# Kernel optimization log

Hardware: AMD Instinct MI355X
Metric: run time of the kernel (lower is better)

## Reference

```python
import jax, jax.numpy as jnp
import numpy as np
import math

NUM_HEADS = 12


def setup_inputs() -> dict:
    key = jax.random.key(0)
    ks = jax.random.split(key, 9)
    R, L, B, E = 128, 512, 1, 768
    s = 1.0 / math.sqrt(E)
    return {
        "x": jax.random.normal(ks[0], (R, L, B, E), dtype=jnp.float32),
        "wq": jax.random.normal(ks[1], (E, E), dtype=jnp.float32) * s,
        "bq": jax.random.normal(ks[2], (E,), dtype=jnp.float32) * 0.02,
        "wk": jax.random.normal(ks[3], (E, E), dtype=jnp.float32) * s,
        "bk": jax.random.normal(ks[4], (E,), dtype=jnp.float32) * 0.02,
        "wv": jax.random.normal(ks[5], (E, E), dtype=jnp.float32) * s,
        "bv": jax.random.normal(ks[6], (E,), dtype=jnp.float32) * 0.02,
        "wo": jax.random.normal(ks[7], (E, E), dtype=jnp.float32) * s,
        "bo": jax.random.normal(ks[8], (E,), dtype=jnp.float32) * 0.02,
    }


def reference(x, wq, bq, wk, bk, wv, bv, wo, bo):
    # x: [num_rows, num_cols, batch, embed_dim]
    R, L, B, E = x.shape
    H = NUM_HEADS
    D = E // H
    # scaling = head_dim**-0.5 / sqrt(num_rows)  (align_scaling)
    scaling = (D ** -0.5) / math.sqrt(R)

    q = (x @ wq.T + bq).reshape(R, L, B, H, D) * scaling
    k = (x @ wk.T + bk).reshape(R, L, B, H, D)
    v = (x @ wv.T + bv).reshape(R, L, B, H, D)

    # row attention: contract over rows r and head_dim d -> logits [h, n, i, j]
    attn_weights = jnp.einsum("rinhd,rjnhd->hnij", q, k)
    attn_probs = jax.nn.softmax(attn_weights, axis=-1)

    context = jnp.einsum("hnij,rjnhd->rinhd", attn_probs, v)
    context = context.reshape(R, L, B, E)
    output = context @ wo.T + bo
    return (output, attn_probs)
```

## Files before the change

kernel.cpp:

```cpp
#include <hip/hip_runtime.h>
#include <hip/hip_bf16.h>

typedef unsigned short u16;
typedef u16   u16x4 __attribute__((ext_vector_type(4)));
typedef u16   u16x8 __attribute__((ext_vector_type(8)));
typedef short bf16x8 __attribute__((ext_vector_type(8)));
typedef float f32x4 __attribute__((ext_vector_type(4)));

#define R_    128
#define L_    512
#define E_    768
#define H_    12
#define RD_   8192
#define M_    65536
#define OUT0_N 50331648
#define PART_ 3145728

__device__ __forceinline__ u16 rne_bf16(float f) {
  unsigned u = __builtin_bit_cast(unsigned, f);
  u += 0x7FFFu + ((u >> 16) & 1u);
  return (u16)(u >> 16);
}

__device__ __forceinline__ void gload_lds16(const u16* g, u16* l) {
  __builtin_amdgcn_global_load_lds(
      (const __attribute__((address_space(1))) void*)g,
      (__attribute__((address_space(3))) void*)l, 16, 0, 0);
}

__device__ __forceinline__ int xcd_remap(int d, int nwg) {
  return (d & 7) * (nwg >> 3) + (d >> 3);
}

__device__ __forceinline__ void gemm_core(
    const u16* __restrict__ Ab, const u16* __restrict__ Bb,
    const int lda, const int ldb, const int K,
    u16* sm, f32x4 acc[4][4])
{
  const int t    = threadIdx.x;
  const int lane = t & 63;
  const int w    = t >> 6;
  const int wm   = (w >> 1) << 6;
  const int wn   = (w & 1) << 6;
  const int frow = lane & 15;

  const int srow = (w << 3) + (lane >> 3);
  const int scol = ((lane & 7) ^ (lane >> 3)) << 3;
  const u16* gA = Ab + (size_t)srow * lda + scol;
  const u16* gB = Bb + (size_t)srow * ldb + scol;
  const int stg_l = (w << 9) + (lane << 3);

#pragma unroll
  for (int j = 0; j < 4; ++j) {
    gload_lds16(gA + (size_t)(j << 5) * lda, sm + (j << 11) + stg_l);
    gload_lds16(gB + (size_t)(j << 5) * ldb, sm + 8192 + (j << 11) + stg_l);
  }

  const int nt = K >> 6;
  for (int tt = 0; tt < nt; ++tt) {
    const int cur = tt & 1;
    u16* bufc = sm + (cur << 14);
    u16* bufn = sm + ((cur ^ 1) << 14);
    __builtin_amdgcn_s_barrier();
    if (tt + 1 < nt) {
      const u16* gA1 = gA + ((size_t)(tt + 1) << 6);
      const u16* gB1 = gB + ((size_t)(tt + 1) << 6);
#pragma unroll
      for (int j = 0; j < 4; ++j) {
        gload_lds16(gA1 + (size_t)(j << 5) * lda, bufn + (j << 11) + stg_l);
        gload_lds16(gB1 + (size_t)(j << 5) * ldb, bufn + 8192 + (j << 11) + stg_l);
      }
      asm volatile("s_waitcnt vmcnt(8)" ::: "memory");
    } else {
      asm volatile("s_waitcnt vmcnt(0)" ::: "memory");
    }
    __builtin_amdgcn_s_barrier();
    const u16* sA = bufc;
    const u16* sB = bufc + 8192;
#pragma unroll
    for (int kk = 0; kk < 2; ++kk) {
      const int rdcol = (((kk << 2) + (lane >> 4)) ^ (lane & 7)) << 3;
      bf16x8 af[4], bff[4];
#pragma unroll
      for (int a = 0; a < 4; ++a)
        af[a] = *(const bf16x8*)(sA + ((wm + a * 16 + frow) << 6) + rdcol);
#pragma unroll
      for (int b = 0; b < 4; ++b)
        bff[b] = *(const bf16x8*)(sB + ((wn + b * 16 + frow) << 6) + rdcol);
#pragma unroll
      for (int a = 0; a < 4; ++a)
#pragma unroll
        for (int b = 0; b < 4; ++b)
          acc[a][b] = __builtin_amdgcn_mfma_f32_16x16x32_bf16(af[a], bff[b], acc[a][b], 0, 0, 0);
    }
  }
}

#define EPILOGUE_IDX                              \
  const int lane = threadIdx.x & 63;              \
  const int w    = threadIdx.x >> 6;              \
  const int wm   = (w >> 1) << 6;                 \
  const int wn   = (w & 1) << 6;                  \
  const int row4 = (lane >> 4) << 2;              \
  const int coll = lane & 15;

#define ACC_INIT                                  \
  f32x4 acc[4][4];                                \
  {                                               \
    f32x4 zz = {0.0f, 0.0f, 0.0f, 0.0f};          \
    _Pragma("unroll")                             \
    for (int a = 0; a < 4; ++a)                   \
      _Pragma("unroll")                           \
      for (int b = 0; b < 4; ++b) acc[a][b] = zz; \
  }

__global__ __launch_bounds__(256) void k_gemm_qkv(
    const u16* __restrict__ xbf, const u16* __restrict__ wqkv,
    const float* __restrict__ bq, const float* __restrict__ bk,
    const float* __restrict__ bv,
    u16* __restrict__ qt, u16* __restrict__ kt, u16* __restrict__ vt2,
    const float scaling)
{
  __shared__ __align__(16) u16 smem[32768];
  const int d0 = blockIdx.x + 18 * blockIdx.y;
  const int l  = xcd_remap(d0, 18 * 512);
  const int bn = l % 18;
  const int bm = l / 18;
  ACC_INIT;
  gemm_core(xbf + (size_t)bm * 128 * E_, wqkv + (size_t)bn * 128 * E_,
            E_, E_, E_, smem, acc);
  EPILOGUE_IDX;
  const int n0 = bn * 128;
  const int which = n0 / E_;
  const int c0 = n0 - which * E_;
  const float* bias = (which == 0) ? bq : (which == 1) ? bk : bv;

  if (which < 2) {
    u16* dst = (which == 0) ? qt : kt;
    const float mult = (which == 0) ? scaling : 1.0f;
#pragma unroll
    for (int a = 0; a < 4; ++a) {
#pragma unroll
      for (int b = 0; b < 4; ++b) {
        const int nl = wn + b * 16 + coll;
        const int c = c0 + nl;
        const int h = c >> 6, d = c & 63;
        const float bias_v = bias[c];
#pragma unroll
        for (int r = 0; r < 4; ++r) {
          const int m = bm * 128 + wm + a * 16 + row4 + r;
          const int rr = m >> 9, i = m & 511;
          const float v = (acc[a][b][r] + bias_v) * mult;
          dst[((size_t)(h * 512 + i) << 13) + (rr << 6) + d] = rne_bf16(v);
        }
      }
    }
  } else {
    __syncthreads();
    u16* Tr = smem;
#pragma unroll
    for (int a = 0; a < 4; ++a) {
      const int mlb = wm + a * 16 + row4;
#pragma unroll
      for (int b = 0; b < 4; ++b) {
        const int nl = wn + b * 16 + coll;
        const float bias_v = bias[c0 + nl];
        u16x4 pk;
#pragma unroll
        for (int r = 0; r < 4; ++r) pk[r] = rne_bf16(acc[a][b][r] + bias_v);
        *(u16x4*)(Tr + nl * 136 + mlb) = pk;
      }
    }
    __syncthreads();
    const int rr = (bm * 128) >> 9;
    const int j0 = (bm * 128) & 511;
    for (int idx = threadIdx.x; idx < 128 * 16; idx += 256) {
      const int nl = idx >> 4, seg = idx & 15;
      const int c = c0 + nl;
      const int h = c >> 6, d = c & 63;
      u16x8 vdat = *(const u16x8*)(Tr + nl * 136 + (seg << 3));
      *(u16x8*)(vt2 + ((size_t)((h << 13) + (rr << 6) + d) << 9) + j0 + (seg << 3)) = vdat;
    }
  }
}

__global__ __launch_bounds__(256) void k_gemm_logits(
    const u16* __restrict__ qt, const u16* __restrict__ kt,
    float* __restrict__ lgp)
{
  __shared__ __align__(16) u16 smem[32768];
  const int d0 = blockIdx.x + 4 * blockIdx.y + 16 * blockIdx.z;
  const int l  = xcd_remap(d0, 768);
  const int bm = l & 3, bn = (l >> 2) & 3;
  const int hk = l >> 4;
  const int h  = hk >> 2, ks = hk & 3;
  ACC_INIT;
  const u16* A = qt + ((size_t)h << 22) + ((size_t)bm << 20) + (ks << 11);
  const u16* B = kt + ((size_t)h << 22) + ((size_t)bn << 20) + (ks << 11);
  gemm_core(A, B, RD_, RD_, 2048, smem, acc);
  EPILOGUE_IDX;
  float* dst = lgp + ((size_t)(ks * 12 + h) << 18);
#pragma unroll
  for (int a = 0; a < 4; ++a)
#pragma unroll
    for (int b = 0; b < 4; ++b) {
      const int j = bn * 128 + wn + b * 16 + coll;
#pragma unroll
      for (int r = 0; r < 4; ++r) {
        const int i = bm * 128 + wm + a * 16 + row4 + r;
        dst[((size_t)i << 9) + j] = acc[a][b][r];
      }
    }
}

__global__ __launch_bounds__(256) void k_softmax(
    const float* __restrict__ lgp, float* __restrict__ probs,
    u16* __restrict__ pbf)
{
  const int row = blockIdx.x;
  const size_t base = (size_t)row << 9;
  const int t = threadIdx.x;
  const int lane = t & 63, w = t >> 6;
  float x0 = (lgp[base + t]       + lgp[PART_ + base + t])
           + (lgp[2 * (size_t)PART_ + base + t]       + lgp[3 * (size_t)PART_ + base + t]);
  float x1 = (lgp[base + t + 256] + lgp[PART_ + base + t + 256])
           + (lgp[2 * (size_t)PART_ + base + t + 256] + lgp[3 * (size_t)PART_ + base + t + 256]);
  float m = fmaxf(x0, x1);
#pragma unroll
  for (int off = 32; off > 0; off >>= 1) m = fmaxf(m, __shfl_xor(m, off, 64));
  __shared__ float red[8];
  if (lane == 0) red[w] = m;
  __syncthreads();
  m = fmaxf(fmaxf(red[0], red[1]), fmaxf(red[2], red[3]));
  float e0 = __expf(x0 - m), e1 = __expf(x1 - m);
  float s = e0 + e1;
#pragma unroll
  for (int off = 32; off > 0; off >>= 1) s += __shfl_xor(s, off, 64);
  if (lane == 0) red[4 + w] = s;
  __syncthreads();
  s = (red[4] + red[5]) + (red[6] + red[7]);
  const float inv = 1.0f / s;
  const float p0 = e0 * inv, p1 = e1 * inv;
  probs[base + t] = p0;
  probs[base + t + 256] = p1;
  pbf[base + t]       = rne_bf16(p0);
  pbf[base + t + 256] = rne_bf16(p1);
}

__global__ __launch_bounds__(256) void k_gemm_ctx(
    const u16* __restrict__ pbf, const u16* __restrict__ vt2,
    u16* __restrict__ ctx)
{
  __shared__ __align__(16) u16 smem[32768];
  const int d0 = blockIdx.x + 4 * blockIdx.y + 256 * blockIdx.z;
  const int l  = xcd_remap(d0, 3072);
  const int bm = l & 3, bn = (l >> 2) & 63, h = l >> 8;
  ACC_INIT;
  const u16* A = pbf + ((size_t)h << 18) + ((size_t)bm << 16);
  const u16* B = vt2 + ((size_t)h << 22) + ((size_t)bn << 16);
  gemm_core(A, B, 512, 512, 512, smem, acc);
  EPILOGUE_IDX;
#pragma unroll
  for (int a = 0; a < 4; ++a)
#pragma unroll
    for (int b = 0; b < 4; ++b) {
      const int n = bn * 128 + wn + b * 16 + coll;
      const int rr = n >> 6, d = n & 63;
#pragma unroll
      for (int r = 0; r < 4; ++r) {
        const int i = bm * 128 + wm + a * 16 + row4 + r;
        ctx[(size_t)(rr * 512 + i) * E_ + (h << 6) + d] = rne_bf16(acc[a][b][r]);
      }
    }
}

__global__ __launch_bounds__(256) void k_gemm_out(
    const u16* __restrict__ ctx, const u16* __restrict__ wob,
    const float* __restrict__ bo, float* __restrict__ out0)
{
  __shared__ __align__(16) u16 smem[32768];
  const int d0 = blockIdx.x + 6 * blockIdx.y;
  const int l  = xcd_remap(d0, 3072);
  const int bn = l % 6;
  const int bm = l / 6;
  ACC_INIT;
  gemm_core(ctx + (size_t)bm * 128 * E_, wob + (size_t)bn * 128 * E_,
            E_, E_, E_, smem, acc);
  EPILOGUE_IDX;
#pragma unroll
  for (int a = 0; a < 4; ++a)
#pragma unroll
    for (int b = 0; b < 4; ++b) {
      const int n = bn * 128 + wn + b * 16 + coll;
      const float bias_v = bo[n];
#pragma unroll
      for (int r = 0; r < 4; ++r) {
        const int m = bm * 128 + wm + a * 16 + row4 + r;
        out0[(size_t)m * E_ + n] = acc[a][b][r] + bias_v;
      }
    }
}

__device__ __forceinline__ u16x4 cvt4(float4 v) {
  u16x4 o;
  o.x = rne_bf16(v.x); o.y = rne_bf16(v.y);
  o.z = rne_bf16(v.z); o.w = rne_bf16(v.w);
  return o;
}

__global__ __launch_bounds__(256) void k_cvt_x(
    const float4* __restrict__ src, u16x4* __restrict__ dst, const int n4)
{
  const int stride = gridDim.x * blockDim.x;
  for (int i = blockIdx.x * blockDim.x + threadIdx.x; i < n4; i += stride)
    dst[i] = cvt4(src[i]);
}

__global__ __launch_bounds__(256) void k_cvt_w(
    const float4* __restrict__ wq, const float4* __restrict__ wk,
    const float4* __restrict__ wv, const float4* __restrict__ wo,
    u16x4* __restrict__ wqkv, u16x4* __restrict__ wob)
{
  const int n4 = (E_ * E_) / 4;
  const int stride = gridDim.x * blockDim.x;
  for (int i = blockIdx.x * blockDim.x + threadIdx.x; i < n4; i += stride) {
    wqkv[i]            = cvt4(wq[i]);
    wqkv[n4 + i]       = cvt4(wk[i]);
    wqkv[2 * n4 + i]   = cvt4(wv[i]);
    wob[i]             = cvt4(wo[i]);
  }
}

__global__ void k_ws_too_small(float* out0) {
  if (threadIdx.x == 0 && blockIdx.x == 0) out0[0] = 1.0e9f;
}

extern "C" void kernel_launch(void* const* d_in, const int* in_sizes, int n_in,
                              void* d_out, int out_size, void* d_ws, size_t ws_size,
                              hipStream_t stream)
{
  const float* x  = (const float*)d_in[0];
  const float* wq = (const float*)d_in[1];
  const float* bq = (const float*)d_in[2];
  const float* wk = (const float*)d_in[3];
  const float* bk = (const float*)d_in[4];
  const float* wv = (const float*)d_in[5];
  const float* bv = (const float*)d_in[6];
  const float* wo = (const float*)d_in[7];
  const float* bo = (const float*)d_in[8];

  float* out0 = (float*)d_out;
  float* outp = out0 + (size_t)OUT0_N;

  const size_t off_xbf   = 0;
  const size_t off_qt    = 100663296;
  const size_t off_kt    = 201326592;
  const size_t off_vt    = 301989888;
  const size_t off_pbf   = 402653184;
  const size_t off_wqkv  = 408944640;
  const size_t off_wob   = 412483584;
  const size_t need      = 413663232;

  if (ws_size < need) {
    k_ws_too_small<<<1, 64, 0, stream>>>(out0);
    return;
  }

  char* ws = (char*)d_ws;
  u16* xbf  = (u16*)(ws + off_xbf);
  float* lgp = (float*)(ws + off_xbf);
  u16* qt   = (u16*)(ws + off_qt);
  u16* kt   = (u16*)(ws + off_kt);
  u16* vt2  = (u16*)(ws + off_vt);
  u16* pbf  = (u16*)(ws + off_pbf);
  u16* wqkv = (u16*)(ws + off_wqkv);
  u16* wob  = (u16*)(ws + off_wob);

  const float scaling = 0.011048543456039806f;

  k_cvt_x<<<2048, 256, 0, stream>>>((const float4*)x, (u16x4*)xbf, OUT0_N / 4);
  k_cvt_w<<<192, 256, 0, stream>>>((const float4*)wq, (const float4*)wk,
                                   (const float4*)wv, (const float4*)wo,
                                   (u16x4*)wqkv, (u16x4*)wob);
  k_gemm_qkv<<<dim3(18, 512), 256, 0, stream>>>(xbf, wqkv, bq, bk, bv,
                                                qt, kt, vt2, scaling);
  k_gemm_logits<<<dim3(4, 4, 48), 256, 0, stream>>>(qt, kt, lgp);
  k_softmax<<<6144, 256, 0, stream>>>(lgp, outp, pbf);
  k_gemm_ctx<<<dim3(4, 64, 12), 256, 0, stream>>>(pbf, vt2, xbf );
  k_gemm_out<<<dim3(6, 512), 256, 0, stream>>>(xbf, wob, bo, out0);
}
```

Baseline: 666.7 us.

## Use 256x256 tiles with 8 waves and triple-buffered LDS for projection and context GEMMs

Adds a new GEMM core that computes 256x256 output tiles with 512 threads (8 waves, 128x64 per wave), a BK of 32 and three LDS stages with an XOR swizzle. The QKV, context and output projection kernels are switched to it with their grids halved in each dimension. The V transpose epilogue now runs in two passes through LDS. The larger tiles are meant to raise arithmetic intensity and cut global and LDS traffic per FLOP, at the cost of more accumulator registers, fewer blocks and lower occupancy.

New measurement: 617.8 us. 1.08x faster.

```diff
diff --git a/kernel.cpp b/kernel.cpp
--- a/kernel.cpp
+++ b/kernel.cpp
@@ -31,6 +31,89 @@
 __device__ __forceinline__ int xcd_remap(int d, int nwg) {
   return (d & 7) * (nwg >> 3) + (d >> 3);
 }
+
+__device__ __forceinline__ void gemm_core256(
+    const u16* __restrict__ Ab, const u16* __restrict__ Bb,
+    const int lda, const int ldb, const int K,
+    u16* sm, f32x4 acc[8][4])
+{
+  const int t    = threadIdx.x;
+  const int lane = t & 63;
+  const int w    = t >> 6;
+  const int wm   = (w >> 2) << 7;
+  const int wn   = (w & 3) << 6;
+  const int frow = lane & 15;
+
+  const int srow  = t >> 2;
+  const int gslot = (t & 3) ^ ((t >> 3) & 3);
+  const u16* gA0 = Ab + (size_t)srow * lda + (gslot << 3);
+  const u16* gA1 = Ab + (size_t)(srow + 128) * lda + (gslot << 3);
+  const u16* gB0 = Bb + (size_t)srow * ldb + (gslot << 3);
+  const u16* gB1 = Bb + (size_t)(srow + 128) * ldb + (gslot << 3);
+  const int stg = t << 3;
+
+  const int rdoff = (((lane >> 4) ^ ((lane >> 1) & 3)) << 3);
+
+#define STAGE256(tt_, buf_)                                            \
+  {                                                                    \
+    const size_t ko_ = (size_t)(tt_) << 5;                             \
+    gload_lds16(gA0 + ko_, (buf_) + stg);                              \
+    gload_lds16(gA1 + ko_, (buf_) + 4096 + stg);                       \
+    gload_lds16(gB0 + ko_, (buf_) + 8192 + stg);                       \
+    gload_lds16(gB1 + ko_, (buf_) + 12288 + stg);                      \
+  }
+
+  const int nt = K >> 5;
+  STAGE256(0, sm);
+  if (nt > 1) STAGE256(1, sm + 16384);
+  asm volatile("s_waitcnt vmcnt(4)" ::: "memory");
+  __builtin_amdgcn_s_barrier();
+
+  for (int tt = 0; tt < nt; ++tt) {
+    u16* bufc = sm + (tt % 3) * 16384;
+    const bool st = (tt + 2 < nt);
+    if (st) STAGE256(tt + 2, sm + ((tt + 2) % 3) * 16384);
+
+    bf16x8 af[8], bff[4];
+#pragma unroll
+    for (int b = 0; b < 4; ++b)
+      bff[b] = *(const bf16x8*)(bufc + 8192 + ((wn + b * 16 + frow) << 5) + rdoff);
+#pragma unroll
+    for (int a = 0; a < 8; ++a)
+      af[a] = *(const bf16x8*)(bufc + ((wm + a * 16 + frow) << 5) + rdoff);
+
+    __builtin_amdgcn_s_setprio(1);
+#pragma unroll
+    for (int a = 0; a < 8; ++a)
+#pragma unroll
+      for (int b = 0; b < 4; ++b)
+        acc[a][b] = __builtin_amdgcn_mfma_f32_16x16x32_bf16(af[a], bff[b], acc[a][b], 0, 0, 0);
+    __builtin_amdgcn_s_setprio(0);
+
+    if (st) asm volatile("s_waitcnt vmcnt(4)" ::: "memory");
+    else    asm volatile("s_waitcnt vmcnt(0)" ::: "memory");
+    __builtin_amdgcn_s_barrier();
+  }
+#undef STAGE256
+}
+
+#define EPILOGUE_IDX256                           \
+  const int lane = threadIdx.x & 63;              \
+  const int w    = threadIdx.x >> 6;              \
+  const int wm   = (w >> 2) << 7;                 \
+  const int wn   = (w & 3) << 6;                  \
+  const int row4 = (lane >> 4) << 2;              \
+  const int coll = lane & 15;
+
+#define ACC_INIT256                               \
+  f32x4 acc[8][4];                                \
+  {                                               \
+    f32x4 zz = {0.0f, 0.0f, 0.0f, 0.0f};          \
+    _Pragma("unroll")                             \
+    for (int a = 0; a < 8; ++a)                   \
+      _Pragma("unroll")                           \
+      for (int b = 0; b < 4; ++b) acc[a][b] = zz; \
+  }
 
 __device__ __forceinline__ void gemm_core(
     const u16* __restrict__ Ab, const u16* __restrict__ Bb,
@@ -114,41 +197,39 @@
       for (int b = 0; b < 4; ++b) acc[a][b] = zz; \
   }
 
-__global__ __launch_bounds__(256) void k_gemm_qkv(
+__global__ __launch_bounds__(512) void k_gemm_qkv(
     const u16* __restrict__ xbf, const u16* __restrict__ wqkv,
     const float* __restrict__ bq, const float* __restrict__ bk,
     const float* __restrict__ bv,
     u16* __restrict__ qt, u16* __restrict__ kt, u16* __restrict__ vt2,
     const float scaling)
 {
-  __shared__ __align__(16) u16 smem[32768];
-  const int d0 = blockIdx.x + 18 * blockIdx.y;
-  const int l  = xcd_remap(d0, 18 * 512);
-  const int bn = l % 18;
-  const int bm = l / 18;
-  ACC_INIT;
-  gemm_core(xbf + (size_t)bm * 128 * E_, wqkv + (size_t)bn * 128 * E_,
-            E_, E_, E_, smem, acc);
-  EPILOGUE_IDX;
-  const int n0 = bn * 128;
-  const int which = n0 / E_;
-  const int c0 = n0 - which * E_;
+  __shared__ __align__(16) u16 smem[49152];
+  const int d0 = blockIdx.x + 9 * blockIdx.y;
+  const int l  = xcd_remap(d0, 2304);
+  const int bn = l % 9;
+  const int bm = l / 9;
+  ACC_INIT256;
+  gemm_core256(xbf + (size_t)bm * 256 * E_, wqkv + (size_t)bn * 256 * E_,
+               E_, E_, E_, smem, acc);
+  EPILOGUE_IDX256;
+  const int which = bn / 3;
+  const int c0 = (bn % 3) << 8;
   const float* bias = (which == 0) ? bq : (which == 1) ? bk : bv;
 
   if (which < 2) {
     u16* dst = (which == 0) ? qt : kt;
     const float mult = (which == 0) ? scaling : 1.0f;
 #pragma unroll
-    for (int a = 0; a < 4; ++a) {
+    for (int a = 0; a < 8; ++a) {
 #pragma unroll
       for (int b = 0; b < 4; ++b) {
-        const int nl = wn + b * 16 + coll;
-        const int c = c0 + nl;
+        const int c = c0 + wn + b * 16 + coll;
         const int h = c >> 6, d = c & 63;
         const float bias_v = bias[c];
 #pragma unroll
         for (int r = 0; r < 4; ++r) {
-          const int m = bm * 128 + wm + a * 16 + row4 + r;
+          const int m = (bm << 8) + wm + a * 16 + row4 + r;
           const int rr = m >> 9, i = m & 511;
           const float v = (acc[a][b][r] + bias_v) * mult;
           dst[((size_t)(h * 512 + i) << 13) + (rr << 6) + d] = rne_bf16(v);
@@ -156,30 +237,35 @@
       }
     }
   } else {
-    __syncthreads();
-    u16* Tr = smem;
-#pragma unroll
-    for (int a = 0; a < 4; ++a) {
-      const int mlb = wm + a * 16 + row4;
-#pragma unroll
-      for (int b = 0; b < 4; ++b) {
-        const int nl = wn + b * 16 + coll;
-        const float bias_v = bias[c0 + nl];
-        u16x4 pk;
-#pragma unroll
-        for (int r = 0; r < 4; ++r) pk[r] = rne_bf16(acc[a][b][r] + bias_v);
-        *(u16x4*)(Tr + nl * 136 + mlb) = pk;
-      }
-    }
-    __syncthreads();
-    const int rr = (bm * 128) >> 9;
-    const int j0 = (bm * 128) & 511;
-    for (int idx = threadIdx.x; idx < 128 * 16; idx += 256) {
-      const int nl = idx >> 4, seg = idx & 15;
-      const int c = c0 + nl;
-      const int h = c >> 6, d = c & 63;
-      u16x8 vdat = *(const u16x8*)(Tr + nl * 136 + (seg << 3));
-      *(u16x8*)(vt2 + ((size_t)((h << 13) + (rr << 6) + d) << 9) + j0 + (seg << 3)) = vdat;
+    const int rr = bm >> 1;
+    const int j0 = (bm & 1) << 8;
+    const int wc2 = (w & 3) >> 1;
+    for (int p = 0; p < 2; ++p) {
+      __syncthreads();
+      if (wc2 == p) {
+#pragma unroll
+        for (int a = 0; a < 8; ++a) {
+          const int ml = wm + a * 16 + row4;
+#pragma unroll
+          for (int b = 0; b < 4; ++b) {
+            const int c = c0 + wn + b * 16 + coll;
+            const int nl = (wn + b * 16 + coll) - (p << 7);
+            const float bias_v = bias[c];
+            u16x4 pk;
+#pragma unroll
+            for (int r = 0; r < 4; ++r) pk[r] = rne_bf16(acc[a][b][r] + bias_v);
+            *(u16x4*)(smem + nl * 264 + ml) = pk;
+          }
+        }
+      }
+      __syncthreads();
+      for (int idx = threadIdx.x; idx < 4096; idx += 512) {
+        const int nl = idx >> 5, seg = idx & 31;
+        const int c = c0 + (p << 7) + nl;
+        const int h = c >> 6, d = c & 63;
+        u16x8 vdat = *(const u16x8*)(smem + nl * 264 + (seg << 3));
+        *(u16x8*)(vt2 + ((size_t)((h << 13) + (rr << 6) + d) << 9) + j0 + (seg << 3)) = vdat;
+      }
     }
   }
 }
@@ -247,55 +333,55 @@
   pbf[base + t + 256] = rne_bf16(p1);
 }
 
-__global__ __launch_bounds__(256) void k_gemm_ctx(
+__global__ __launch_bounds__(512) void k_gemm_ctx(
     const u16* __restrict__ pbf, const u16* __restrict__ vt2,
     u16* __restrict__ ctx)
 {
-  __shared__ __align__(16) u16 smem[32768];
-  const int d0 = blockIdx.x + 4 * blockIdx.y + 256 * blockIdx.z;
-  const int l  = xcd_remap(d0, 3072);
-  const int bm = l & 3, bn = (l >> 2) & 63, h = l >> 8;
-  ACC_INIT;
-  const u16* A = pbf + ((size_t)h << 18) + ((size_t)bm << 16);
-  const u16* B = vt2 + ((size_t)h << 22) + ((size_t)bn << 16);
-  gemm_core(A, B, 512, 512, 512, smem, acc);
-  EPILOGUE_IDX;
-#pragma unroll
-  for (int a = 0; a < 4; ++a)
+  __shared__ __align__(16) u16 smem[49152];
+  const int d0 = blockIdx.x + (blockIdx.y << 6);
+  const int l  = xcd_remap(d0, 768);
+  const int bm = l & 1, bn = (l >> 1) & 31, h = l >> 6;
+  ACC_INIT256;
+  const u16* A = pbf + ((size_t)h << 18) + ((size_t)bm << 17);
+  const u16* B = vt2 + ((size_t)h << 22) + ((size_t)bn << 17);
+  gemm_core256(A, B, 512, 512, 512, smem, acc);
+  EPILOGUE_IDX256;
+#pragma unroll
+  for (int a = 0; a < 8; ++a)
 #pragma unroll
     for (int b = 0; b < 4; ++b) {
-      const int n = bn * 128 + wn + b * 16 + coll;
+      const int n = (bn << 8) + wn + b * 16 + coll;
       const int rr = n >> 6, d = n & 63;
 #pragma unroll
       for (int r = 0; r < 4; ++r) {
-        const int i = bm * 128 + wm + a * 16 + row4 + r;
-        ctx[(size_t)(rr * 512 + i) * E_ + (h << 6) + d] = rne_bf16(acc[a][b][r]);
-      }
-    }
-}
-
-__global__ __launch_bounds__(256) void k_gemm_out(
+        const int i = (bm << 8) + wm + a * 16 + row4 + r;
+        ctx[(size_t)((rr << 9) + i) * E_ + (h << 6) + d] = rne_bf16(acc[a][b][r]);
+      }
+    }
+}
+
+__global__ __launch_bounds__(512) void k_gemm_out(
     const u16* __restrict__ ctx, const u16* __restrict__ wob,
     const float* __restrict__ bo, float* __restrict__ out0)
 {
-  __shared__ __align__(16) u16 smem[32768];
-  const int d0 = blockIdx.x + 6 * blockIdx.y;
-  const int l  = xcd_remap(d0, 3072);
-  const int bn = l % 6;
-  const int bm = l / 6;
-  ACC_INIT;
-  gemm_core(ctx + (size_t)bm * 128 * E_, wob + (size_t)bn * 128 * E_,
-            E_, E_, E_, smem, acc);
-  EPILOGUE_IDX;
-#pragma unroll
-  for (int a = 0; a < 4; ++a)
+  __shared__ __align__(16) u16 smem[49152];
+  const int d0 = blockIdx.x + 3 * blockIdx.y;
+  const int l  = xcd_remap(d0, 768);
+  const int bn = l % 3;
+  const int bm = l / 3;
+  ACC_INIT256;
+  gemm_core256(ctx + (size_t)bm * 256 * E_, wob + (size_t)bn * 256 * E_,
+               E_, E_, E_, smem, acc);
+  EPILOGUE_IDX256;
+#pragma unroll
+  for (int a = 0; a < 8; ++a)
 #pragma unroll
     for (int b = 0; b < 4; ++b) {
-      const int n = bn * 128 + wn + b * 16 + coll;
+      const int n = (bn << 8) + wn + b * 16 + coll;
       const float bias_v = bo[n];
 #pragma unroll
       for (int r = 0; r < 4; ++r) {
-        const int m = bm * 128 + wm + a * 16 + row4 + r;
+        const int m = (bm << 8) + wm + a * 16 + row4 + r;
         out0[(size_t)m * E_ + n] = acc[a][b][r] + bias_v;
       }
     }
@@ -382,10 +468,10 @@
   k_cvt_w<<<192, 256, 0, stream>>>((const float4*)wq, (const float4*)wk,
                                    (const float4*)wv, (const float4*)wo,
                                    (u16x4*)wqkv, (u16x4*)wob);
-  k_gemm_qkv<<<dim3(18, 512), 256, 0, stream>>>(xbf, wqkv, bq, bk, bv,
-                                                qt, kt, vt2, scaling);
+  k_gemm_qkv<<<dim3(9, 256), 512, 0, stream>>>(xbf, wqkv, bq, bk, bv,
+                                               qt, kt, vt2, scaling);
   k_gemm_logits<<<dim3(4, 4, 48), 256, 0, stream>>>(qt, kt, lgp);
   k_softmax<<<6144, 256, 0, stream>>>(lgp, outp, pbf);
-  k_gemm_ctx<<<dim3(4, 64, 12), 256, 0, stream>>>(pbf, vt2, xbf );
-  k_gemm_out<<<dim3(6, 512), 256, 0, stream>>>(xbf, wob, bo, out0);
-}
+  k_gemm_ctx<<<dim3(64, 12), 512, 0, stream>>>(pbf, vt2, xbf );
+  k_gemm_out<<<dim3(3, 256), 512, 0, stream>>>(xbf, wob, bo, out0);
+}
```
